# Performance work log

Measured on AMD Instinct MI355X. Metric: run time of the kernel, lower is better.

## Reference

```python
import jax, jax.numpy as jnp
import numpy as np

B, D, E, H = 4, 128, 512, 512

def setup_inputs() -> dict:
    key = jax.random.key(0)
    k1, k2, k3, k4, k5 = jax.random.split(key, 5)
    s = 1.0 / np.sqrt(H)
    return {
        "x_decoder": jax.random.normal(k1, (B, D, H), dtype=jnp.float32),
        "x_encoder": jax.random.normal(k2, (B, E, H), dtype=jnp.float32),
        "mask": jnp.zeros((B, E), dtype=bool),
        "W1": jax.random.uniform(k3, (H, H), jnp.float32, -s, s),  # nn.Linear weight (out,in)
        "W2": jax.random.uniform(k4, (H, H), jnp.float32, -s, s),
        "v": jax.random.uniform(k5, (H,), jnp.float32, -s, s),     # Linear(H,1) weight squeezed
    }

def reference(x_decoder, x_encoder, mask, W1, W2, v):
    # w1(x_encoder): (B,E,H); w2(x_decoder): (B,D,H)
    enc_t = jnp.einsum('beh,oh->beo', x_encoder, W1)
    dec_t = jnp.einsum('bdh,oh->bdo', x_decoder, W2)
    # additive attention: tanh over broadcast sum (B,D,E,H), reduce with v -> (B,D,E)
    prod = jnp.einsum('bdeh,h->bde', jnp.tanh(dec_t[:, :, None, :] + enc_t[:, None, :, :]), v)
    prod = jnp.where(mask[:, None, :], -jnp.inf, prod)
    return jax.nn.log_softmax(prod, axis=-1)
```

## Files before the change

kernel.cpp:

```cpp
#include <hip/hip_runtime.h>
#include <math.h>

#define BATCH 4
#define DDIM  128
#define EDIM  512
#define HDIM  512

#define TANH_SCALE 2.8853900817779268f

typedef short short8v __attribute__((ext_vector_type(8)));
typedef float f32x4   __attribute__((ext_vector_type(4)));
typedef float f32x2   __attribute__((ext_vector_type(2)));

#define EXP2F(x) __builtin_amdgcn_exp2f(x)
#define RCPF(x)  __builtin_amdgcn_rcpf(x)

static __device__ inline unsigned short f2bf(float f) {
    unsigned u = __float_as_uint(f);
    return (unsigned short)((u + 0x7FFFu + ((u >> 16) & 1u)) >> 16);
}
static __device__ inline unsigned pack_bf2(float f0, float f1) {
    unsigned u0 = __float_as_uint(f0), u1 = __float_as_uint(f1);
    u0 += 0x7FFFu + ((u0 >> 16) & 1u);
    u1 += 0x7FFFu + ((u1 >> 16) & 1u);
    return __builtin_amdgcn_perm(u1, u0, 0x07060302u);
}
static __device__ inline float bf2f(unsigned short h) {
    return __uint_as_float(((unsigned)h) << 16);
}

__global__ __launch_bounds__(256)
void gemm_both(const float* __restrict__ xdec, const float* __restrict__ W2,
               const float* __restrict__ xenc, const float* __restrict__ W1,
               unsigned short* __restrict__ P, unsigned short* __restrict__ Q) {
    __shared__ unsigned short As[2][64][40];
    __shared__ unsigned short Bs[2][64][40];

    const int id = blockIdx.x;
    const float *Ab, *Bb;
    unsigned short* Cb;
    int m0, n0;
    if (id < 64) {
        int b = id >> 4, r = id & 15;
        m0 = (r >> 3) * 64; n0 = (r & 7) * 64;
        Ab = xdec + (long)b * DDIM * HDIM;
        Bb = W2;
        Cb = P + (long)b * DDIM * HDIM;
    } else {
        int t2 = id - 64;
        int b = t2 >> 6, r = t2 & 63;
        m0 = (r >> 3) * 64; n0 = (r & 7) * 64;
        Ab = W1;
        Bb = xenc + (long)b * EDIM * HDIM;
        Cb = Q + (long)b * HDIM * EDIM;
    }

    const int t    = threadIdx.x;
    const int srow = t >> 2;
    const int skq  = (t & 3) << 3;

    const int wid = t >> 6, wm = wid >> 1, wn = wid & 1;
    const int l   = t & 63, lr = l & 15, c16 = l >> 4;

    f32x4 acc[2][2] = {};

    const float* ap = Ab + (long)(m0 + srow) * HDIM + skq;
    const float* bp = Bb + (long)(n0 + srow) * HDIM + skq;

    float4 a0 = *(const float4*)ap, a1 = *(const float4*)(ap + 4);
    float4 b0 = *(const float4*)bp, b1 = *(const float4*)(bp + 4);

    int cur = 0;
    for (int k0 = 0; k0 < HDIM; k0 += 32) {
        uint4 apk, bpk;
        apk.x = pack_bf2(a0.x, a0.y); apk.y = pack_bf2(a0.z, a0.w);
        apk.z = pack_bf2(a1.x, a1.y); apk.w = pack_bf2(a1.z, a1.w);
        bpk.x = pack_bf2(b0.x, b0.y); bpk.y = pack_bf2(b0.z, b0.w);
        bpk.z = pack_bf2(b1.x, b1.y); bpk.w = pack_bf2(b1.z, b1.w);
        *(uint4*)&As[cur][srow][skq] = apk;
        *(uint4*)&Bs[cur][srow][skq] = bpk;

        if (k0 + 32 < HDIM) {
            ap += 32; bp += 32;
            a0 = *(const float4*)ap; a1 = *(const float4*)(ap + 4);
            b0 = *(const float4*)bp; b1 = *(const float4*)(bp + 4);
        }

        asm volatile("s_waitcnt lgkmcnt(0)" ::: "memory");
        __builtin_amdgcn_s_barrier();
        __builtin_amdgcn_sched_barrier(0);

        short8v af[2], bf[2];
        #pragma unroll
        for (int fm = 0; fm < 2; ++fm)
            af[fm] = *(const short8v*)&As[cur][wm * 32 + fm * 16 + lr][c16 * 8];
        #pragma unroll
        for (int fn = 0; fn < 2; ++fn)
            bf[fn] = *(const short8v*)&Bs[cur][wn * 32 + fn * 16 + lr][c16 * 8];
        #pragma unroll
        for (int fm = 0; fm < 2; ++fm)
            #pragma unroll
            for (int fn = 0; fn < 2; ++fn)
                acc[fm][fn] = __builtin_amdgcn_mfma_f32_16x16x32_bf16(
                    af[fm], bf[fn], acc[fm][fn], 0, 0, 0);
        cur ^= 1;
    }

    const int crow = c16 << 2;
    #pragma unroll
    for (int fm = 0; fm < 2; ++fm)
        #pragma unroll
        for (int fn = 0; fn < 2; ++fn)
            #pragma unroll
            for (int r = 0; r < 4; ++r) {
                int rr = m0 + wm * 32 + fm * 16 + crow + r;
                int cc = n0 + wn * 32 + fn * 16 + lr;
                Cb[(long)rr * 512 + cc] = f2bf(EXP2F(TANH_SCALE * acc[fm][fn][r]));
            }
}

__global__ __launch_bounds__(512)
void attn_partial(const unsigned short* __restrict__ P,
                  const unsigned short* __restrict__ Q,
                  const float* __restrict__ vw,
                  float* __restrict__ partial) {
    const int g     = blockIdx.x;
    const int xcd   = g & 7;
    const int b     = xcd & 3;
    const int idx   = g >> 3;
    const int chunk = idx & 3;
    const int dp    = (idx >> 2) + ((xcd >> 2) << 5);
    const int pair  = b * 64 + dp;
    const int bd0   = pair * 2;
    const int t     = threadIdx.x;
    const int eq    = t & 127;
    const int hg    = t >> 7;
    const int h0    = chunk * 128;

    __shared__ f32x2 combo2[64][3];
    __shared__ float lds[4][128][9];

    if (t < 64) {
        int h = h0 + t * 2;
        f32x2 p0, p1, vv;
        p0.x = bf2f(P[bd0 * HDIM + h]);       p0.y = bf2f(P[bd0 * HDIM + h + 1]);
        p1.x = bf2f(P[(bd0 + 1) * HDIM + h]); p1.y = bf2f(P[(bd0 + 1) * HDIM + h + 1]);
        vv.x = -2.0f * vw[h];                 vv.y = -2.0f * vw[h + 1];
        combo2[t][0] = p0; combo2[t][1] = p1; combo2[t][2] = vv;
    }
    __syncthreads();

    const unsigned short* qb =
        Q + b * HDIM * EDIM + (h0 + hg * 32) * EDIM + eq * 4;
    float a00 = 0.f, a01 = 0.f, a02 = 0.f, a03 = 0.f;
    float a10 = 0.f, a11 = 0.f, a12 = 0.f, a13 = 0.f;
    f32x2 ones; ones.x = 1.0f; ones.y = 1.0f;

#define PAIR_SET(Pp, q0p, q1p, VV, accA, accB)                                  \
    {                                                                           \
        f32x2 xp, yp, den, tt, num;                                             \
        asm("v_pk_fma_f32 %0, %1, %2, %3 op_sel_hi:[0,1,1]"                     \
            : "=v"(xp) : "v"(Pp), "v"(q0p), "v"(ones));                         \
        asm("v_pk_fma_f32 %0, %1, %2, %3 op_sel:[1,0,0] op_sel_hi:[1,1,1]"      \
            : "=v"(yp) : "v"(Pp), "v"(q1p), "v"(ones));                         \
        asm("v_pk_mul_f32 %0, %1, %2" : "=v"(den) : "v"(xp), "v"(yp));          \
        asm("v_pk_mul_f32 %0, %1, %2 op_sel:[1,0] op_sel_hi:[1,1]"              \
            : "=v"(tt) : "v"(VV), "v"(xp));                                     \
        asm("v_pk_fma_f32 %0, %1, %2, %3 op_sel_hi:[0,1,1]"                     \
            : "=v"(num) : "v"(VV), "v"(yp), "v"(tt));                           \
        accA = fmaf(num.x, RCPF(den.x), accA);                                  \
        accB = fmaf(num.y, RCPF(den.y), accB);                                  \
    }

    #pragma unroll 4
    for (int ii = 0; ii < 16; ++ii) {
        uint2 qv0 = *(const uint2*)(qb + (size_t)(2 * ii) * EDIM);
        uint2 qv1 = *(const uint2*)(qb + (size_t)(2 * ii + 1) * EDIM);
        f32x2 P0 = combo2[hg * 16 + ii][0];
        f32x2 P1 = combo2[hg * 16 + ii][1];
        f32x2 VV = combo2[hg * 16 + ii][2];
        f32x2 qA0, qB0, qA1, qB1;
        qA0.x = __uint_as_float(qv0.x << 16);
        qA0.y = __uint_as_float(qv0.x & 0xffff0000u);
        qB0.x = __uint_as_float(qv0.y << 16);
        qB0.y = __uint_as_float(qv0.y & 0xffff0000u);
        qA1.x = __uint_as_float(qv1.x << 16);
        qA1.y = __uint_as_float(qv1.x & 0xffff0000u);
        qB1.x = __uint_as_float(qv1.y << 16);
        qB1.y = __uint_as_float(qv1.y & 0xffff0000u);

        PAIR_SET(P0, qA0, qA1, VV, a00, a01);
        PAIR_SET(P0, qB0, qB1, VV, a02, a03);
        PAIR_SET(P1, qA0, qA1, VV, a10, a11);
        PAIR_SET(P1, qB0, qB1, VV, a12, a13);
    }
#undef PAIR_SET

    float* myl = &lds[hg][eq][0];
    myl[0] = a00; myl[1] = a01; myl[2] = a02; myl[3] = a03;
    myl[4] = a10; myl[5] = a11; myl[6] = a12; myl[7] = a13;
    __syncthreads();

    float* pp = partial + ((size_t)pair * 4 + chunk) * 1024;
    #pragma unroll
    for (int rp = 0; rp < 2; ++rp) {
        int pos = t + rp * 512;
        int d = pos >> 9, e = pos & 511;
        int j = d * 4 + (e & 3), eqi = e >> 2;
        float v = (lds[0][eqi][j] + lds[1][eqi][j]) +
                  (lds[2][eqi][j] + lds[3][eqi][j]);
        pp[pos] = v;
    }
}

__global__ __launch_bounds__(512)
void lsm_final(const float* __restrict__ partial,
               const unsigned char* __restrict__ mask,
               float* __restrict__ out) {
    const int pair = blockIdx.x;
    const int b    = pair >> 6;
    const int bd0  = pair * 2;
    const int e    = threadIdx.x;

    __shared__ float red0[8], red1[8];

    const float* pp = partial + (size_t)pair * 4096;
    float acc0 = (pp[e]        + pp[1024 + e]) + (pp[2048 + e] + pp[3072 + e]);
    float acc1 = (pp[512 + e]  + pp[1536 + e]) + (pp[2560 + e] + pp[3584 + e]);

    const bool mk = mask[b * EDIM + e];
    float val0 = mk ? -INFINITY : acc0;
    float val1 = mk ? -INFINITY : acc1;

    const int wid = e >> 6, lid = e & 63;

    float m0 = val0, m1 = val1;
    #pragma unroll
    for (int o = 32; o >= 1; o >>= 1) {
        m0 = fmaxf(m0, __shfl_xor(m0, o));
        m1 = fmaxf(m1, __shfl_xor(m1, o));
    }
    if (lid == 0) { red0[wid] = m0; red1[wid] = m1; }
    __syncthreads();
    m0 = red0[0]; m1 = red1[0];
    #pragma unroll
    for (int i = 1; i < 8; ++i) { m0 = fmaxf(m0, red0[i]); m1 = fmaxf(m1, red1[i]); }
    __syncthreads();

    float s0 = __expf(val0 - m0), s1 = __expf(val1 - m1);
    #pragma unroll
    for (int o = 32; o >= 1; o >>= 1) {
        s0 += __shfl_xor(s0, o);
        s1 += __shfl_xor(s1, o);
    }
    if (lid == 0) { red0[wid] = s0; red1[wid] = s1; }
    __syncthreads();
    float tot0 = 0.f, tot1 = 0.f;
    #pragma unroll
    for (int i = 0; i < 8; ++i) { tot0 += red0[i]; tot1 += red1[i]; }

    out[(long)bd0 * EDIM + e]       = val0 - m0 - __logf(tot0);
    out[(long)(bd0 + 1) * EDIM + e] = val1 - m1 - __logf(tot1);
}

extern "C" void kernel_launch(void* const* d_in, const int* in_sizes, int n_in,
                              void* d_out, int out_size, void* d_ws, size_t ws_size,
                              hipStream_t stream) {
    const float*         xdec = (const float*)d_in[0];
    const float*         xenc = (const float*)d_in[1];
    const unsigned char* mask = (const unsigned char*)d_in[2];
    const float*         W1   = (const float*)d_in[3];
    const float*         W2   = (const float*)d_in[4];
    const float*         vw   = (const float*)d_in[5];
    float*               out  = (float*)d_out;

    unsigned short* P = (unsigned short*)d_ws;
    unsigned short* Q = P + 262144;
    float* partial    = (float*)(Q + 1048576);

    gemm_both<<<320, 256, 0, stream>>>(xdec, W2, xenc, W1, P, Q);
    attn_partial<<<1024, 512, 0, stream>>>(P, Q, vw, partial);
    lsm_final<<<256, 512, 0, stream>>>(partial, mask, out);
}
```

Measured before the change: 33.77 us.

## Fuse attention partial sums and log-softmax into one full-H kernel

Each block now covers the full H dimension for a decoder pair using 1024 threads in 8 h-groups, then reduces in LDS and computes the masked log-softmax in place. This removes the partial-sum buffer round trip through global memory and one kernel launch. In exchange, the grid drops from 1024 blocks to 256 blocks of 1024 threads, which lowers parallelism and may reduce occupancy and latency hiding on the attention stage.

```diff
diff --git a/kernel.cpp b/kernel.cpp
--- a/kernel.cpp
+++ b/kernel.cpp
@@ -119,29 +119,28 @@
             }
 }
 
-__global__ __launch_bounds__(512)
-void attn_partial(const unsigned short* __restrict__ P,
-                  const unsigned short* __restrict__ Q,
-                  const float* __restrict__ vw,
-                  float* __restrict__ partial) {
-    const int g     = blockIdx.x;
-    const int xcd   = g & 7;
-    const int b     = xcd & 3;
-    const int idx   = g >> 3;
-    const int chunk = idx & 3;
-    const int dp    = (idx >> 2) + ((xcd >> 2) << 5);
-    const int pair  = b * 64 + dp;
-    const int bd0   = pair * 2;
-    const int t     = threadIdx.x;
-    const int eq    = t & 127;
-    const int hg    = t >> 7;
-    const int h0    = chunk * 128;
-
-    __shared__ f32x2 combo2[64][3];
-    __shared__ float lds[4][128][9];
-
-    if (t < 64) {
-        int h = h0 + t * 2;
+__global__ __launch_bounds__(1024)
+void attn_lsm(const unsigned short* __restrict__ P,
+              const unsigned short* __restrict__ Q,
+              const unsigned char* __restrict__ mask,
+              const float* __restrict__ vw,
+              float* __restrict__ out) {
+    const int g    = blockIdx.x;
+    const int xcd  = g & 7;
+    const int b    = xcd & 3;
+    const int dp   = (g >> 3) + ((xcd >> 2) << 5);
+    const int pair = b * 64 + dp;
+    const int bd0  = pair * 2;
+    const int t    = threadIdx.x;
+    const int eq   = t & 127;
+    const int hg   = t >> 7;
+
+    __shared__ f32x2 combo2[256][3];
+    __shared__ float lds[8][128][9];
+    __shared__ float red[16];
+
+    if (t < 256) {
+        int h = t * 2;
         f32x2 p0, p1, vv;
         p0.x = bf2f(P[bd0 * HDIM + h]);       p0.y = bf2f(P[bd0 * HDIM + h + 1]);
         p1.x = bf2f(P[(bd0 + 1) * HDIM + h]); p1.y = bf2f(P[(bd0 + 1) * HDIM + h + 1]);
@@ -150,8 +149,7 @@
     }
     __syncthreads();
 
-    const unsigned short* qb =
-        Q + b * HDIM * EDIM + (h0 + hg * 32) * EDIM + eq * 4;
+    const unsigned short* qb = Q + b * HDIM * EDIM + (hg * 64) * EDIM + eq * 4;
     float a00 = 0.f, a01 = 0.f, a02 = 0.f, a03 = 0.f;
     float a10 = 0.f, a11 = 0.f, a12 = 0.f, a13 = 0.f;
     f32x2 ones; ones.x = 1.0f; ones.y = 1.0f;
@@ -173,12 +171,12 @@
     }
 
     #pragma unroll 4
-    for (int ii = 0; ii < 16; ++ii) {
+    for (int ii = 0; ii < 32; ++ii) {
         uint2 qv0 = *(const uint2*)(qb + (size_t)(2 * ii) * EDIM);
         uint2 qv1 = *(const uint2*)(qb + (size_t)(2 * ii + 1) * EDIM);
-        f32x2 P0 = combo2[hg * 16 + ii][0];
-        f32x2 P1 = combo2[hg * 16 + ii][1];
-        f32x2 VV = combo2[hg * 16 + ii][2];
+        f32x2 P0 = combo2[hg * 32 + ii][0];
+        f32x2 P1 = combo2[hg * 32 + ii][1];
+        f32x2 VV = combo2[hg * 32 + ii][2];
         f32x2 qA0, qB0, qA1, qB1;
         qA0.x = __uint_as_float(qv0.x << 16);
         qA0.y = __uint_as_float(qv0.x & 0xffff0000u);
@@ -201,66 +199,38 @@
     myl[4] = a10; myl[5] = a11; myl[6] = a12; myl[7] = a13;
     __syncthreads();
 
-    float* pp = partial + ((size_t)pair * 4 + chunk) * 1024;
-    #pragma unroll
-    for (int rp = 0; rp < 2; ++rp) {
-        int pos = t + rp * 512;
-        int d = pos >> 9, e = pos & 511;
-        int j = d * 4 + (e & 3), eqi = e >> 2;
-        float v = (lds[0][eqi][j] + lds[1][eqi][j]) +
-                  (lds[2][eqi][j] + lds[3][eqi][j]);
-        pp[pos] = v;
-    }
-}
-
-__global__ __launch_bounds__(512)
-void lsm_final(const float* __restrict__ partial,
-               const unsigned char* __restrict__ mask,
-               float* __restrict__ out) {
-    const int pair = blockIdx.x;
-    const int b    = pair >> 6;
-    const int bd0  = pair * 2;
-    const int e    = threadIdx.x;
-
-    __shared__ float red0[8], red1[8];
-
-    const float* pp = partial + (size_t)pair * 4096;
-    float acc0 = (pp[e]        + pp[1024 + e]) + (pp[2048 + e] + pp[3072 + e]);
-    float acc1 = (pp[512 + e]  + pp[1536 + e]) + (pp[2560 + e] + pp[3584 + e]);
+    const int d = t >> 9, e = t & 511;
+    const int j = d * 4 + (e & 3), eqi = e >> 2;
+    float acc = ((lds[0][eqi][j] + lds[1][eqi][j]) +
+                 (lds[2][eqi][j] + lds[3][eqi][j])) +
+                ((lds[4][eqi][j] + lds[5][eqi][j]) +
+                 (lds[6][eqi][j] + lds[7][eqi][j]));
 
     const bool mk = mask[b * EDIM + e];
-    float val0 = mk ? -INFINITY : acc0;
-    float val1 = mk ? -INFINITY : acc1;
-
-    const int wid = e >> 6, lid = e & 63;
-
-    float m0 = val0, m1 = val1;
-    #pragma unroll
-    for (int o = 32; o >= 1; o >>= 1) {
-        m0 = fmaxf(m0, __shfl_xor(m0, o));
-        m1 = fmaxf(m1, __shfl_xor(m1, o));
-    }
-    if (lid == 0) { red0[wid] = m0; red1[wid] = m1; }
-    __syncthreads();
-    m0 = red0[0]; m1 = red1[0];
-    #pragma unroll
-    for (int i = 1; i < 8; ++i) { m0 = fmaxf(m0, red0[i]); m1 = fmaxf(m1, red1[i]); }
-    __syncthreads();
-
-    float s0 = __expf(val0 - m0), s1 = __expf(val1 - m1);
-    #pragma unroll
-    for (int o = 32; o >= 1; o >>= 1) {
-        s0 += __shfl_xor(s0, o);
-        s1 += __shfl_xor(s1, o);
-    }
-    if (lid == 0) { red0[wid] = s0; red1[wid] = s1; }
-    __syncthreads();
-    float tot0 = 0.f, tot1 = 0.f;
-    #pragma unroll
-    for (int i = 0; i < 8; ++i) { tot0 += red0[i]; tot1 += red1[i]; }
-
-    out[(long)bd0 * EDIM + e]       = val0 - m0 - __logf(tot0);
-    out[(long)(bd0 + 1) * EDIM + e] = val1 - m1 - __logf(tot1);
+    float val = mk ? -INFINITY : acc;
+
+    const int wv = t >> 6, lid = t & 63, dg8 = d * 8;
+
+    float m = val;
+    #pragma unroll
+    for (int o = 32; o >= 1; o >>= 1) m = fmaxf(m, __shfl_xor(m, o));
+    if (lid == 0) red[wv] = m;
+    __syncthreads();
+    m = red[dg8];
+    #pragma unroll
+    for (int i = 1; i < 8; ++i) m = fmaxf(m, red[dg8 + i]);
+    __syncthreads();
+
+    float s = __expf(val - m);
+    #pragma unroll
+    for (int o = 32; o >= 1; o >>= 1) s += __shfl_xor(s, o);
+    if (lid == 0) red[wv] = s;
+    __syncthreads();
+    float tot = 0.f;
+    #pragma unroll
+    for (int i = 0; i < 8; ++i) tot += red[dg8 + i];
+
+    out[(long)(bd0 + d) * EDIM + e] = val - m - __logf(tot);
 }
 
 extern "C" void kernel_launch(void* const* d_in, const int* in_sizes, int n_in,
@@ -276,9 +246,7 @@
 
     unsigned short* P = (unsigned short*)d_ws;
     unsigned short* Q = P + 262144;
-    float* partial    = (float*)(Q + 1048576);
 
     gemm_both<<<320, 256, 0, stream>>>(xdec, W2, xenc, W1, P, Q);
-    attn_partial<<<1024, 512, 0, stream>>>(P, Q, vw, partial);
-    lsm_final<<<256, 512, 0, stream>>>(partial, mask, out);
-}
+    attn_lsm<<<256, 1024, 0, stream>>>(P, Q, mask, vw, out);
+}
```

New measurement: 30.61 us, median of 2. -9.4%, faster.
